# Kernel optimization log

Measured on AMD Instinct MI355X. Metric: run time of the kernel, lower is better.

## Reference

```python
import jax, jax.numpy as jnp
import numpy as np

B, NL, L1, D = 16, 12, 197, 768   # batch, num_layers, 1+num_patches, embed_dim
E, K, C, IMG = 4, 3, 21, 224      # num_experts, topk, num_classes, image_size


def setup_inputs() -> dict:
    key = jax.random.key(0)
    k0, k1, k2 = jax.random.split(key, 3)
    features = jax.random.normal(k0, (B, NL, L1, D), jnp.float32)
    gate_W = jax.random.normal(k1, (D, E), jnp.float32) / np.sqrt(D).astype(np.float32)
    gate_b = jnp.zeros((E,), jnp.float32)
    expert_W = jax.random.normal(k2, (E, D, C), jnp.float32) / np.sqrt(D).astype(np.float32)
    expert_b = jnp.zeros((E, C), jnp.float32)
    return dict(features=features, gate_W=gate_W, gate_b=gate_b,
                expert_W=expert_W, expert_b=expert_b)


def reference(features, gate_W, gate_b, expert_W, expert_b):
    cls_tokens = features[:, :, 0, :]          # [B, NL, D]
    feats = features[:, :, 1:, :]              # [B, NL, L, D]
    gate_score = cls_tokens @ gate_W + gate_b  # [B, NL, E]
    gate_prob = jax.nn.softmax(gate_score.transpose(0, 2, 1), axis=-1)  # [B, E, NL]
    # per-expert topk over layers (vectorized over experts)
    topv, topi = jax.lax.top_k(gate_prob, K)   # [B, E, K]
    # gather selected layer feature maps: [B, E, K, L, D]
    gathered = jnp.take_along_axis(feats[:, None], topi[:, :, :, None, None], axis=2)
    w = jax.nn.softmax(topv, axis=-1)          # re-softmax of topk values, [B, E, K]
    mixed = jnp.einsum('bek,bekld->beld', w, gathered)  # [B, E, L, D]
    # expert heads (UPerNet modeled as linear decode + bilinear upsample)
    logits = jnp.einsum('beld,edc->belc', mixed, expert_W) + expert_b[None, :, None, :]
    L = logits.shape[2]
    g = int(np.sqrt(L))                        # 14x14 patch grid
    logits = logits.reshape(B, E, g, g, C).transpose(0, 1, 4, 2, 3)  # [B,E,C,g,g]
    logits = jax.image.resize(logits, (B, E, C, IMG, IMG), method='bilinear')
    return logits.mean(axis=1)                 # mean over experts -> [B, C, IMG, IMG]
```

## Files before the change

kernel.cpp:

```cpp
#include <hip/hip_runtime.h>
#include <math.h>

#define B_ 16
#define NL_ 12
#define L1_ 197
#define D_ 768
#define E_ 4
#define K_ 3
#define C_ 21
#define IMG_ 224
#define LP_ 196
#define NJ_ 84
#define MT_ 52
#define KSTEPS 24

typedef __attribute__((ext_vector_type(8))) short short8;
typedef __attribute__((ext_vector_type(4))) float f32x4;
typedef unsigned short ushort_t;

__device__ __forceinline__ ushort_t bf16rne(float x) {
    unsigned u = __float_as_uint(x);
    unsigned r = (u + 0x7FFFu + ((u >> 16) & 1u)) >> 16;
    return (ushort_t)r;
}

__device__ __forceinline__ void glds16(const void* g, void* l) {
    __builtin_amdgcn_global_load_lds(
        (const __attribute__((address_space(1))) unsigned int*)g,
        (__attribute__((address_space(3))) unsigned int*)l, 16, 0, 0);
}

__device__ __forceinline__ void select_be(const float* __restrict__ gs, int b, int e,
                                          int idx[3], float w[3]) {
    float p[NL_]; float mx = -1e30f;
    #pragma unroll
    for (int nl = 0; nl < NL_; ++nl) { float v = gs[(b * NL_ + nl) * E_ + e]; p[nl] = v; mx = fmaxf(mx, v); }
    float ss = 0.f;
    #pragma unroll
    for (int nl = 0; nl < NL_; ++nl) { p[nl] = expf(p[nl] - mx); ss += p[nl]; }
    float inv = 1.0f / ss;
    #pragma unroll
    for (int nl = 0; nl < NL_; ++nl) p[nl] *= inv;
    unsigned used = 0; float v[3];
    #pragma unroll
    for (int k = 0; k < 3; ++k) {
        float best = -1.f; int bi = 0;
        #pragma unroll
        for (int nl = 0; nl < NL_; ++nl)
            if (!((used >> nl) & 1u) && p[nl] > best) { best = p[nl]; bi = nl; }
        used |= 1u << bi; idx[k] = bi; v[k] = best;
    }
    float x1 = expf(v[1] - v[0]), x2 = expf(v[2] - v[0]);
    float isw = 1.0f / (1.0f + x1 + x2);
    w[0] = isw; w[1] = x1 * isw; w[2] = x2 * isw;
}

__global__ __launch_bounds__(256) void prep_kernel(
        const float* __restrict__ feat, const float* __restrict__ gW,
        const float* __restrict__ gb, const float* __restrict__ eW,
        ushort_t* __restrict__ WtB, float* __restrict__ gs) {
    int blk = blockIdx.x, t = threadIdx.x;
    if (blk < B_ * NL_) {
        if (t < 64) {
            const float* cls = feat + (size_t)blk * L1_ * D_;
            float a0 = 0.f, a1 = 0.f, a2 = 0.f, a3 = 0.f;
            for (int q = 0; q < D_ / 64; ++q) {
                int d = t + 64 * q;
                float x = cls[d];
                float4 w = *(const float4*)(gW + (size_t)d * E_);
                a0 += x * w.x; a1 += x * w.y; a2 += x * w.z; a3 += x * w.w;
            }
            for (int off = 32; off > 0; off >>= 1) {
                a0 += __shfl_down(a0, off); a1 += __shfl_down(a1, off);
                a2 += __shfl_down(a2, off); a3 += __shfl_down(a3, off);
            }
            if (t == 0) {
                gs[blk * E_ + 0] = a0 + gb[0]; gs[blk * E_ + 1] = a1 + gb[1];
                gs[blk * E_ + 2] = a2 + gb[2]; gs[blk * E_ + 3] = a3 + gb[3];
            }
        }
    } else {
        int j = blk - B_ * NL_;
        if (j < NJ_) {
            int e = j / C_, c = j % C_;
            for (int k = t; k < D_; k += 256)
                WtB[(size_t)j * D_ + k] = bf16rne(eW[((size_t)e * D_ + k) * C_ + c]);
        } else {
            for (int k = t; k < D_; k += 256) WtB[(size_t)j * D_ + k] = 0;
        }
    }
}

__global__ __launch_bounds__(256) void select_kernel(
        const float* __restrict__ gs, int* __restrict__ topi,
        float* __restrict__ wgt, int* __restrict__ list, int* __restrict__ nsel) {
    __shared__ int sidx[B_ * E_ * 3];
    __shared__ int wcnt[3];
    int t = threadIdx.x;
    if (t < B_ * E_) {
        int b = t >> 2, e = t & 3;
        int idx[3]; float w[3];
        select_be(gs, b, e, idx, w);
        #pragma unroll
        for (int k = 0; k < 3; ++k) {
            topi[t * 3 + k] = idx[k]; wgt[t * 3 + k] = w[k]; sidx[t * 3 + k] = idx[k];
        }
    }
    __syncthreads();
    int f = 0, rank = 0;
    if (t < B_ * NL_) {
        int b = t / NL_, nl = t % NL_;
        #pragma unroll
        for (int ek = 0; ek < 12; ++ek) f |= (sidx[b * 12 + ek] == nl);
        unsigned long long m = __ballot(f != 0);
        int lane = t & 63;
        rank = __popcll(m & ((1ull << lane) - 1ull));
        if (lane == 0) wcnt[t >> 6] = __popcll(m);
    }
    __syncthreads();
    if (t < B_ * NL_ && f) {
        int wv = t >> 6;
        int base = 0;
        if (wv > 0) base += wcnt[0];
        if (wv > 1) base += wcnt[1];
        list[base + rank] = t;
    }
    if (t == 0) nsel[0] = wcnt[0] + wcnt[1] + wcnt[2];
}

__global__ __launch_bounds__(256, 4) void gemm_kernel(
        const float* __restrict__ feat, const ushort_t* __restrict__ WtB,
        const int* __restrict__ list, const int* __restrict__ nsel,
        float* __restrict__ proj) {
    int blk = blockIdx.x;
    if (blk >= nsel[0] * 4) return;
    int tile = blk & 3;
    int bn = list[blk >> 2];
    int rows_real = min(MT_, LP_ - tile * MT_);

    __shared__ f32x4  As4[2][64 * 8];
    __shared__ short8 Bs[2][96 * 4];

    int t = threadIdx.x;
    int w = t >> 6, lane = t & 63;
    int la = lane & 15, kp = lane >> 4;

    const float* fbase = feat + ((size_t)bn * L1_ + 1 + tile * MT_) * D_;
    int sA0 = w * 128 + lane;
    int sA1 = sA0 + 64;
    int rA0 = sA0 >> 3, qA0 = (sA0 & 7) ^ (rA0 & 7);
    int rA1 = sA1 >> 3, qA1 = (sA1 & 7) ^ (rA1 & 7);
    const float* gA0 = fbase + (size_t)min(rA0, rows_real - 1) * D_ + qA0 * 4;
    const float* gA1 = fbase + (size_t)min(rA1, rows_real - 1) * D_ + qA1 * 4;

    int sB0 = w * 64 + lane;
    int jB0 = sB0 >> 2, cB0 = sB0 & 3;
    int kgB0 = cB0 ^ (jB0 & 3) ^ (((jB0 >> 2) & 1) << 1);
    const ushort_t* gB0 = WtB + (size_t)jB0 * D_ + kgB0 * 8;
    int sB1 = 256 + w * 64 + lane;
    int jB1 = sB1 >> 2, cB1 = sB1 & 3;
    int kgB1 = cB1 ^ (jB1 & 3) ^ (((jB1 >> 2) & 1) << 1);
    const ushort_t* gB1 = WtB + (size_t)jB1 * D_ + kgB1 * 8;
    bool doB1 = (w < 2);

    int arow = w * 16 + la;
    int ar0 = arow * 8 + ((kp * 2) ^ (arow & 7));
    int bidx[6];
    #pragma unroll
    for (int nt = 0; nt < 6; ++nt) {
        int j = nt * 16 + la;
        bidx[nt] = j * 4 + (kp ^ (j & 3) ^ (((j >> 2) & 1) << 1));
    }

    glds16(gA0, &As4[0][w * 128]);
    glds16(gA1, &As4[0][w * 128 + 64]);
    glds16(gB0, &Bs[0][w * 64]);
    if (doB1) glds16(gB1, &Bs[0][256 + w * 64]);
    __syncthreads();

    f32x4 acc[6];
    #pragma unroll
    for (int nt = 0; nt < 6; ++nt) acc[nt] = (f32x4)0.0f;

    for (int s = 0; s < KSTEPS; ++s) {
        int cur = s & 1;
        if (s + 1 < KSTEPS) {
            int k0 = (s + 1) * 32;
            glds16(gA0 + k0, &As4[cur ^ 1][w * 128]);
            glds16(gA1 + k0, &As4[cur ^ 1][w * 128 + 64]);
            glds16(gB0 + k0, &Bs[cur ^ 1][w * 64]);
            if (doB1) glds16(gB1 + k0, &Bs[cur ^ 1][256 + w * 64]);
        }
        {
            f32x4 a0 = As4[cur][ar0];
            f32x4 a1 = As4[cur][ar0 ^ 1];
            short8 af;
            #pragma unroll
            for (int i = 0; i < 4; ++i) {
                af[i]     = (short)bf16rne(a0[i]);
                af[i + 4] = (short)bf16rne(a1[i]);
            }
            #pragma unroll
            for (int nt = 0; nt < 6; ++nt)
                acc[nt] = __builtin_amdgcn_mfma_f32_16x16x32_bf16(
                    af, Bs[cur][bidx[nt]], acc[nt], 0, 0, 0);
        }
        __syncthreads();
    }

    int lr = w * 16 + (kp << 2);
    int l0 = tile * MT_ + lr;
    if (lr < MT_ && l0 < LP_) {
        #pragma unroll
        for (int nt = 0; nt < 6; ++nt) {
            int j = nt * 16 + la;
            if (j < NJ_)
                *(f32x4*)(proj + ((size_t)bn * NJ_ + j) * LP_ + l0) = acc[nt];
        }
    }
}

__global__ __launch_bounds__(256) void upsample_kernel(
        const float* __restrict__ proj, const int* __restrict__ topi,
        const float* __restrict__ wgt, const float* __restrict__ eb,
        float* __restrict__ out) {
    int bq = blockIdx.x;
    int q = bq & 7;
    int bc = bq >> 3;
    int b = bc / C_, c = bc % C_;
    int t = threadIdx.x;
    __shared__ float s[LP_];
    if (t < LP_) {
        float a = 0.25f * (eb[c] + eb[C_ + c] + eb[2 * C_ + c] + eb[3 * C_ + c]);
        #pragma unroll
        for (int e = 0; e < E_; ++e) {
            int base = (b * E_ + e) * 3;
            #pragma unroll
            for (int k = 0; k < 3; ++k) {
                int nl = topi[base + k];
                float wv = 0.25f * wgt[base + k];
                a += wv * proj[(((size_t)b * NL_ + nl) * NJ_ + e * C_ + c) * LP_ + t];
            }
        }
        s[t] = a;
    }
    __syncthreads();
    f32x4* out4 = (f32x4*)out + (size_t)bc * IMG_ * (IMG_ / 4);
    for (int i = t; i < 28 * 56; i += 256) {
        int oy = q * 28 + i / 56;
        int ox4 = (i % 56) * 4;
        float fy = (oy + 0.5f) * 0.0625f - 0.5f;
        fy = fminf(fmaxf(fy, 0.0f), 13.0f);
        int y0 = (int)fy;
        float ty = fy - (float)y0;
        int y1 = min(y0 + 1, 13);
        const float* r0 = s + y0 * 14;
        const float* r1 = s + y1 * 14;
        f32x4 res;
        #pragma unroll
        for (int u = 0; u < 4; ++u) {
            int ox = ox4 + u;
            float fx = (ox + 0.5f) * 0.0625f - 0.5f;
            fx = fminf(fmaxf(fx, 0.0f), 13.0f);
            int x0 = (int)fx;
            float tx = fx - (float)x0;
            int x1 = min(x0 + 1, 13);
            float v00 = r0[x0], v01 = r0[x1];
            float v10 = r1[x0], v11 = r1[x1];
            float top = v00 + tx * (v01 - v00);
            float bot = v10 + tx * (v11 - v10);
            res[u] = top + ty * (bot - top);
        }
        __builtin_nontemporal_store(res, &out4[oy * 56 + (i % 56)]);
    }
}

extern "C" void kernel_launch(void* const* d_in, const int* in_sizes, int n_in,
                              void* d_out, int out_size, void* d_ws, size_t ws_size,
                              hipStream_t stream) {
    const float* feat = (const float*)d_in[0];
    const float* gW   = (const float*)d_in[1];
    const float* gb   = (const float*)d_in[2];
    const float* eW   = (const float*)d_in[3];
    const float* eb   = (const float*)d_in[4];
    float* out = (float*)d_out;

    float* ws = (float*)d_ws;
    float*    gs   = ws;
    int*      topi = (int*)(ws + 768);
    float*    wgt  = ws + 960;
    int*      list = (int*)(ws + 1152);
    int*      nsel = (int*)(ws + 1344);
    ushort_t* WtB  = (ushort_t*)(ws + 1536);
    float*    proj = ws + 38400;

    hipLaunchKernelGGL(prep_kernel, dim3(B_ * NL_ + 96), dim3(256), 0, stream,
                       feat, gW, gb, eW, WtB, gs);
    hipLaunchKernelGGL(select_kernel, dim3(1), dim3(256), 0, stream,
                       gs, topi, wgt, list, nsel);
    hipLaunchKernelGGL(gemm_kernel, dim3(B_ * NL_ * 4), dim3(256), 0, stream,
                       feat, WtB, list, nsel, proj);
    hipLaunchKernelGGL(upsample_kernel, dim3(B_ * C_ * 8), dim3(256), 0, stream,
                       proj, topi, wgt, eb, out);
}
```

Before: 51.40 us.

## Remove select kernel; recompute top-k selection inside gemm and upsample kernels

Drops the single-block select_kernel launch and its serialized dependency step. Each GEMM block now decides from the raw gate scores whether its layer is selected by any expert, ranking by logits since softmax is monotonic. Each upsample block recomputes the per-expert top-k indices and weights into shared memory. This trades one kernel launch and its global round trip for redundant small computations in every block. GEMM block scheduling also becomes sparse, with unselected blocks exiting early instead of being packed by a compacted list.

Measured after the change: 54.10 us. 5.2% more time.

```diff
diff --git a/kernel.cpp b/kernel.cpp
--- a/kernel.cpp
+++ b/kernel.cpp
@@ -53,6 +53,30 @@
     float x1 = expf(v[1] - v[0]), x2 = expf(v[2] - v[0]);
     float isw = 1.0f / (1.0f + x1 + x2);
     w[0] = isw; w[1] = x1 * isw; w[2] = x2 * isw;
+}
+
+__device__ __forceinline__ bool layer_selected(const float* __restrict__ gs,
+                                               int b, int nls) {
+    bool sel = false;
+    #pragma unroll
+    for (int e = 0; e < E_; ++e) {
+        float v[NL_];
+        #pragma unroll
+        for (int nl = 0; nl < NL_; ++nl) v[nl] = gs[(b * NL_ + nl) * E_ + e];
+        int i0 = 0, i1 = 0, i2 = 0; float bv = -1e30f;
+        #pragma unroll
+        for (int nl = 0; nl < NL_; ++nl) if (v[nl] > bv) { bv = v[nl]; i0 = nl; }
+        bv = -1e30f;
+        #pragma unroll
+        for (int nl = 0; nl < NL_; ++nl)
+            if (nl != i0 && v[nl] > bv) { bv = v[nl]; i1 = nl; }
+        bv = -1e30f;
+        #pragma unroll
+        for (int nl = 0; nl < NL_; ++nl)
+            if (nl != i0 && nl != i1 && v[nl] > bv) { bv = v[nl]; i2 = nl; }
+        sel = sel || (i0 == nls) || (i1 == nls) || (i2 == nls);
+    }
+    return sel;
 }
 
 __global__ __launch_bounds__(256) void prep_kernel(
@@ -91,51 +115,13 @@
     }
 }
 
-__global__ __launch_bounds__(256) void select_kernel(
-        const float* __restrict__ gs, int* __restrict__ topi,
-        float* __restrict__ wgt, int* __restrict__ list, int* __restrict__ nsel) {
-    __shared__ int sidx[B_ * E_ * 3];
-    __shared__ int wcnt[3];
-    int t = threadIdx.x;
-    if (t < B_ * E_) {
-        int b = t >> 2, e = t & 3;
-        int idx[3]; float w[3];
-        select_be(gs, b, e, idx, w);
-        #pragma unroll
-        for (int k = 0; k < 3; ++k) {
-            topi[t * 3 + k] = idx[k]; wgt[t * 3 + k] = w[k]; sidx[t * 3 + k] = idx[k];
-        }
-    }
-    __syncthreads();
-    int f = 0, rank = 0;
-    if (t < B_ * NL_) {
-        int b = t / NL_, nl = t % NL_;
-        #pragma unroll
-        for (int ek = 0; ek < 12; ++ek) f |= (sidx[b * 12 + ek] == nl);
-        unsigned long long m = __ballot(f != 0);
-        int lane = t & 63;
-        rank = __popcll(m & ((1ull << lane) - 1ull));
-        if (lane == 0) wcnt[t >> 6] = __popcll(m);
-    }
-    __syncthreads();
-    if (t < B_ * NL_ && f) {
-        int wv = t >> 6;
-        int base = 0;
-        if (wv > 0) base += wcnt[0];
-        if (wv > 1) base += wcnt[1];
-        list[base + rank] = t;
-    }
-    if (t == 0) nsel[0] = wcnt[0] + wcnt[1] + wcnt[2];
-}
-
 __global__ __launch_bounds__(256, 4) void gemm_kernel(
         const float* __restrict__ feat, const ushort_t* __restrict__ WtB,
-        const int* __restrict__ list, const int* __restrict__ nsel,
-        float* __restrict__ proj) {
+        const float* __restrict__ gs, float* __restrict__ proj) {
     int blk = blockIdx.x;
-    if (blk >= nsel[0] * 4) return;
     int tile = blk & 3;
-    int bn = list[blk >> 2];
+    int bn = blk >> 2;
+    if (!layer_selected(gs, bn / NL_, bn % NL_)) return;
     int rows_real = min(MT_, LP_ - tile * MT_);
 
     __shared__ f32x4  As4[2][64 * 8];
@@ -221,25 +207,32 @@
 }
 
 __global__ __launch_bounds__(256) void upsample_kernel(
-        const float* __restrict__ proj, const int* __restrict__ topi,
-        const float* __restrict__ wgt, const float* __restrict__ eb,
-        float* __restrict__ out) {
+        const float* __restrict__ proj, const float* __restrict__ gs,
+        const float* __restrict__ eb, float* __restrict__ out) {
     int bq = blockIdx.x;
     int q = bq & 7;
     int bc = bq >> 3;
     int b = bc / C_, c = bc % C_;
     int t = threadIdx.x;
     __shared__ float s[LP_];
+    __shared__ int   sidx[E_][3];
+    __shared__ float swgt[E_][3];
+    if (t < E_) {
+        int idx[3]; float wv[3];
+        select_be(gs, b, t, idx, wv);
+        #pragma unroll
+        for (int k = 0; k < 3; ++k) { sidx[t][k] = idx[k]; swgt[t][k] = 0.25f * wv[k]; }
+    }
+    __syncthreads();
     if (t < LP_) {
         float a = 0.25f * (eb[c] + eb[C_ + c] + eb[2 * C_ + c] + eb[3 * C_ + c]);
         #pragma unroll
         for (int e = 0; e < E_; ++e) {
-            int base = (b * E_ + e) * 3;
             #pragma unroll
             for (int k = 0; k < 3; ++k) {
-                int nl = topi[base + k];
-                float wv = 0.25f * wgt[base + k];
-                a += wv * proj[(((size_t)b * NL_ + nl) * NJ_ + e * C_ + c) * LP_ + t];
+                int nl = sidx[e][k];
+                a += swgt[e][k] *
+                     proj[(((size_t)b * NL_ + nl) * NJ_ + e * C_ + c) * LP_ + t];
             }
         }
         s[t] = a;
@@ -287,19 +280,13 @@
 
     float* ws = (float*)d_ws;
     float*    gs   = ws;
-    int*      topi = (int*)(ws + 768);
-    float*    wgt  = ws + 960;
-    int*      list = (int*)(ws + 1152);
-    int*      nsel = (int*)(ws + 1344);
     ushort_t* WtB  = (ushort_t*)(ws + 1536);
     float*    proj = ws + 38400;
 
     hipLaunchKernelGGL(prep_kernel, dim3(B_ * NL_ + 96), dim3(256), 0, stream,
                        feat, gW, gb, eW, WtB, gs);
-    hipLaunchKernelGGL(select_kernel, dim3(1), dim3(256), 0, stream,
-                       gs, topi, wgt, list, nsel);
     hipLaunchKernelGGL(gemm_kernel, dim3(B_ * NL_ * 4), dim3(256), 0, stream,
-                       feat, WtB, list, nsel, proj);
+                       feat, WtB, gs, proj);
     hipLaunchKernelGGL(upsample_kernel, dim3(B_ * C_ * 8), dim3(256), 0, stream,
-                       proj, topi, wgt, eb, out);
-}
+                       proj, gs, eb, out);
+}
```
